# Kernel tuning notes

Hardware: AMD Instinct MI355X
Metric: run time of the kernel (lower is better)

The kernel has to match this reference:

```python
import jax, jax.numpy as jnp
import numpy as np

N = 4096      # nodes
DIM = 256     # in/out channels
H = 8         # heads
C = DIM       # per-head channels (PyG TransformerConv: out_channels per head)
EPS = 1e-5    # LayerNorm eps
P_EDGE = 0.01 # adjacency density -> avg in-degree ~41


def setup_inputs() -> dict:
    key = jax.random.key(0)
    ks = jax.random.split(key, 12)
    x = jax.random.normal(ks[0], (1, N, DIM), jnp.float32)
    # sparse random graph encoded densely (dense_to_sparse extracts nonzeros)
    adj_mat = (jax.random.uniform(ks[1], (1, N, N)) < P_EDGE).astype(jnp.float32)
    s = 1.0 / np.sqrt(DIM)
    Wq = jax.random.normal(ks[2], (DIM, H * C), jnp.float32) * s
    Wk = jax.random.normal(ks[3], (DIM, H * C), jnp.float32) * s
    Wv = jax.random.normal(ks[4], (DIM, H * C), jnp.float32) * s
    bq = jax.random.normal(ks[5], (H * C,), jnp.float32) * 0.01
    bk = jax.random.normal(ks[6], (H * C,), jnp.float32) * 0.01
    bv = jax.random.normal(ks[7], (H * C,), jnp.float32) * 0.01
    Wskip = jax.random.normal(ks[8], (DIM, DIM), jnp.float32) * s
    bskip = jax.random.normal(ks[9], (DIM,), jnp.float32) * 0.01
    gamma = jnp.ones((DIM,), jnp.float32)
    beta = jnp.zeros((DIM,), jnp.float32)
    return dict(x=x, adj_mat=adj_mat, Wq=Wq, bq=bq, Wk=Wk, bk=bk, Wv=Wv, bv=bv,
                Wskip=Wskip, bskip=bskip, gamma=gamma, beta=beta)


def reference(x, adj_mat, Wq, bq, Wk, bk, Wv, bv, Wskip, bskip, gamma, beta):
    xs = x[0]            # [N, DIM]
    adj = adj_mat[0]     # [N, N]; adj[j, i] != 0 => edge j -> i (source_to_target)
    q = (xs @ Wq + bq).reshape(N, H, C)
    k = (xs @ Wk + bk).reshape(N, H, C)
    v = (xs @ Wv + bv).reshape(N, H, C)
    # scaled dot-product attention restricted to graph edges
    scores = jnp.einsum('ihc,jhc->hij', q, k) / jnp.sqrt(jnp.float32(C))  # [H,N,N]
    mask = (adj.T != 0.0)[None]  # [1, i_target, j_source]
    neg = jnp.finfo(scores.dtype).min
    attn = jax.nn.softmax(jnp.where(mask, scores, neg), axis=-1)
    # nodes with no in-edges aggregate zero messages (scatter semantics)
    has_nbr = mask.any(axis=-1, keepdims=True)  # [1, N, 1]
    attn = jnp.where(has_nbr, attn, 0.0)
    agg = jnp.einsum('hij,jhc->ihc', attn, v)  # [N, H, C]
    out = agg.mean(axis=1)                      # concat=False -> head mean, [N, DIM]
    out = out + xs @ Wskip + bskip              # root_weight skip connection
    mu = out.mean(axis=-1, keepdims=True)
    var = ((out - mu) ** 2).mean(axis=-1, keepdims=True)
    out = (out - mu) * jax.lax.rsqrt(var + EPS) * gamma + beta  # LayerNorm
    out = out + xs                               # residual
    return out[None]  # [1, N, DIM]
```

## Files before the change

kernel.cpp:

```cpp
#include <hip/hip_runtime.h>
#include <hip/hip_bf16.h>

#define NN   4096
#define DIMM 256
#define HH   8
#define HC   2048
#define CAP  128

#define QSCALE 15.875f
#define SSCALE (0.0625f / (QSCALE * QSCALE))
#define V4SCALE 1.75f
#define V4INV  (4.0f / 7.0f)
#define V4CORR (32.0f / 7.0f)

typedef short    bf16x8 __attribute__((ext_vector_type(8)));
typedef float    f32x4  __attribute__((ext_vector_type(4)));

__device__ __forceinline__ unsigned short f2bf(float f) {
  union { float f; unsigned int u; } un; un.f = f;
  unsigned int r = un.u + 0x7fffu + ((un.u >> 16) & 1u);
  return (unsigned short)(r >> 16);
}
__device__ __forceinline__ int sdot4(unsigned int a, unsigned int b, int c) {
#if __has_builtin(__builtin_amdgcn_sdot4)
  return __builtin_amdgcn_sdot4((int)a, (int)b, c, false);
#else
  c += (int)(signed char)(a)       * (int)(signed char)(b);
  c += (int)(signed char)(a >> 8)  * (int)(signed char)(b >> 8);
  c += (int)(signed char)(a >> 16) * (int)(signed char)(b >> 16);
  c += (int)(signed char)(a >> 24) * (int)(signed char)(b >> 24);
  return c;
#endif
}
__device__ __forceinline__ void gload16(const void* g, void* l) {
  __builtin_amdgcn_global_load_lds(
      (const __attribute__((address_space(1))) unsigned int*)g,
      (__attribute__((address_space(3))) unsigned int*)l, 16, 0, 0);
}
__device__ __forceinline__ unsigned int pack8n(unsigned int a, unsigned int b) {
  const unsigned int ya = a | (a >> 4);
  const unsigned int yb = b | (b >> 4);
  return (ya & 0xFFu) | ((ya >> 8) & 0xFF00u) |
         (((yb & 0xFFu) | ((yb >> 8) & 0xFF00u)) << 16);
}

__global__ __launch_bounds__(256) void build_edges_kernel(
    const float4* __restrict__ adj4, int* __restrict__ deg, int* __restrict__ nbr) {
  const int stride = gridDim.x * blockDim.x;
  for (int e4 = blockIdx.x * blockDim.x + threadIdx.x; e4 < NN * NN / 4; e4 += stride) {
    const float4 a = adj4[e4];
    if (a.x != 0.f || a.y != 0.f || a.z != 0.f || a.w != 0.f) {
      const int e = e4 << 2;
      const int j = e >> 12;
      const int ib = e & (NN - 1);
      if (a.x != 0.f) { int s = atomicAdd(&deg[ib + 0], 1); if (s < CAP) nbr[(ib + 0) * CAP + s] = j; }
      if (a.y != 0.f) { int s = atomicAdd(&deg[ib + 1], 1); if (s < CAP) nbr[(ib + 1) * CAP + s] = j; }
      if (a.z != 0.f) { int s = atomicAdd(&deg[ib + 2], 1); if (s < CAP) nbr[(ib + 2) * CAP + s] = j; }
      if (a.w != 0.f) { int s = atomicAdd(&deg[ib + 3], 1); if (s < CAP) nbr[(ib + 3) * CAP + s] = j; }
    }
  }
}

__global__ __launch_bounds__(128) void sort_nbr_kernel(
    const int* __restrict__ deg, int* __restrict__ nbr) {
  const int i = blockIdx.x, t = threadIdx.x;
  __shared__ int sl[CAP];
  int d = deg[i];
  if (d > CAP) d = CAP;
  if (d <= 1) return;
  sl[t] = (t < d) ? nbr[i * CAP + t] : 0x7fffffff;
  __syncthreads();
  for (int ksz = 2; ksz <= CAP; ksz <<= 1) {
    for (int jsz = ksz >> 1; jsz > 0; jsz >>= 1) {
      const int ixj = t ^ jsz;
      if (ixj > t) {
        const int a = sl[t], b = sl[ixj];
        const bool up = ((t & ksz) == 0);
        if ((up && a > b) || (!up && a < b)) { sl[t] = b; sl[ixj] = a; }
      }
      __syncthreads();
    }
  }
  if (t < d) nbr[i * CAP + t] = sl[t];
}

__global__ __launch_bounds__(256) void cast_x_kernel(
    const float* __restrict__ x, unsigned short* __restrict__ xb) {
  const int gid = blockIdx.x * 256 + threadIdx.x;
  const int m = gid >> 5, c = gid & 31;
  const float4 a = *(const float4*)&x[(size_t)m * 256 + c * 8];
  const float4 b = *(const float4*)&x[(size_t)m * 256 + c * 8 + 4];
  union { unsigned short u[8]; uint4 v; } o;
  o.u[0] = f2bf(a.x); o.u[1] = f2bf(a.y); o.u[2] = f2bf(a.z); o.u[3] = f2bf(a.w);
  o.u[4] = f2bf(b.x); o.u[5] = f2bf(b.y); o.u[6] = f2bf(b.z); o.u[7] = f2bf(b.w);
  const int cs = (c & 24) | ((c & 7) ^ (m & 7));
  *(uint4*)&xb[(size_t)m * 256 + cs * 8] = o.v;
}

__global__ __launch_bounds__(256) void tcast_w_kernel(
    const float* __restrict__ W0, const float* __restrict__ W1,
    const float* __restrict__ W2, unsigned short* __restrict__ T0,
    unsigned short* __restrict__ T1, unsigned short* __restrict__ T2, int Nw) {
  const float* W = blockIdx.z == 0 ? W0 : blockIdx.z == 1 ? W1 : W2;
  unsigned short* T = blockIdx.z == 0 ? T0 : blockIdx.z == 1 ? T1 : T2;
  __shared__ float Tf[64][68];
  const int t = threadIdx.x;
  const int n0 = blockIdx.x * 64, k0 = blockIdx.y * 64;
  const int kk0 = t >> 4, nc = t & 15;
#pragma unroll
  for (int r = 0; r < 4; ++r) {
    const int kk = kk0 + r * 16;
    const float4 a = *(const float4*)&W[(size_t)(k0 + kk) * Nw + n0 + nc * 4];
    Tf[kk][nc * 4 + 0] = a.x; Tf[kk][nc * 4 + 1] = a.y;
    Tf[kk][nc * 4 + 2] = a.z; Tf[kk][nc * 4 + 3] = a.w;
  }
  __syncthreads();
  const int n = t >> 2, cp = t & 3;
#pragma unroll
  for (int qq = 0; qq < 2; ++qq) {
    const int cc = cp * 2 + qq;
    union { unsigned short u[8]; uint4 v; } o;
#pragma unroll
    for (int e = 0; e < 8; ++e) o.u[e] = f2bf(Tf[cc * 8 + e][n]);
    const int ng = n0 + n;
    const int co = cc ^ (ng & 7);
    *(uint4*)&T[(size_t)ng * 256 + blockIdx.y * 64 + co * 8] = o.v;
  }
}

__global__ __launch_bounds__(256) void mfma_gemm_kernel(
    const unsigned short* __restrict__ Abf,
    const unsigned short* __restrict__ B0, const unsigned short* __restrict__ B1,
    const unsigned short* __restrict__ B2, const unsigned short* __restrict__ B3,
    const float* __restrict__ bias0, const float* __restrict__ bias1,
    const float* __restrict__ bias2, const float* __restrict__ bias3,
    void* __restrict__ C0v, void* __restrict__ C1v,
    void* __restrict__ C2v, void* __restrict__ C3v) {
  const int z = blockIdx.z;
  if (z == 3 && blockIdx.x >= 2) return;
  const unsigned short* Bm = z == 0 ? B0 : z == 1 ? B1 : z == 2 ? B2 : B3;
  const float* bias = z == 0 ? bias0 : z == 1 ? bias1 : z == 2 ? bias2 : bias3;
  void* Cv = z == 0 ? C0v : z == 1 ? C1v : z == 2 ? C2v : C3v;
  const int Nc = (z == 3) ? 256 : 2048;

  __shared__ unsigned short lds[2 * 128 * 64];
  unsigned short* As = lds;
  unsigned short* Bs = lds + 128 * 64;

  const int t = threadIdx.x, l = t & 63, w = t >> 6;
  const int m0 = blockIdx.y * 128, n0 = blockIdx.x * 128;
  const int wm = w >> 1, wn = w & 1;

  const f32x4 zero = {0.f, 0.f, 0.f, 0.f};
  f32x4 acc[4][4];
#pragma unroll
  for (int fm = 0; fm < 4; ++fm)
#pragma unroll
    for (int fn = 0; fn < 4; ++fn) acc[fm][fn] = zero;

  for (int kb = 0; kb < 4; ++kb) {
#pragma unroll
    for (int r = 0; r < 4; ++r) {
      const int rr = r * 8 + (l >> 3), ch = l & 7;
      gload16(Abf + (size_t)(m0 + w * 32 + rr) * 256 + kb * 64 + ch * 8,
              As + w * 2048 + r * 512);
      gload16(Bm + (size_t)(n0 + w * 32 + rr) * 256 + kb * 64 + ch * 8,
              Bs + w * 2048 + r * 512);
    }
    __syncthreads();

#pragma unroll
    for (int s = 0; s < 2; ++s) {
      const int chab = (4 * s + (l >> 4)) ^ (l & 7);
      bf16x8 af[4], bfr[4];
#pragma unroll
      for (int fm = 0; fm < 4; ++fm) {
        const int row = wm * 64 + fm * 16 + (l & 15);
        af[fm] = *(const bf16x8*)&As[row * 64 + chab * 8];
      }
#pragma unroll
      for (int fn = 0; fn < 4; ++fn) {
        const int row = wn * 64 + fn * 16 + (l & 15);
        bfr[fn] = *(const bf16x8*)&Bs[row * 64 + chab * 8];
      }
#pragma unroll
      for (int fm = 0; fm < 4; ++fm)
#pragma unroll
        for (int fn = 0; fn < 4; ++fn)
          acc[fm][fn] = __builtin_amdgcn_mfma_f32_16x16x32_bf16(
              af[fm], bfr[fn], acc[fm][fn], 0, 0, 0);
    }
    __syncthreads();
  }

  float bv[4];
#pragma unroll
  for (int fn = 0; fn < 4; ++fn) bv[fn] = bias[n0 + wn * 64 + fn * 16 + (l & 15)];

  if (z < 2) {
    unsigned char* lds8 = (unsigned char*)lds;
    unsigned char* Cc8 = (unsigned char*)Cv;
#pragma unroll
    for (int fm = 0; fm < 4; ++fm) {
      const int col = wn * 64 + (l & 15);
#pragma unroll
      for (int fn = 0; fn < 4; ++fn) {
#pragma unroll
        for (int r = 0; r < 4; ++r) {
          const int row = wm * 64 + fm * 16 + (l >> 4) * 4 + r;
          const float val = acc[fm][fn][r] + bv[fn];
          int vi = (int)rintf(val * QSCALE);
          vi = vi < -127 ? -127 : (vi > 127 ? 127 : vi);
          lds8[row * 128 + col + fn * 16] = (unsigned char)(signed char)vi;
        }
      }
    }
    __syncthreads();
#pragma unroll
    for (int r2 = 0; r2 < 4; ++r2) {
      const int idx = r2 * 256 + t;
      const int row = idx >> 3, colb = (idx & 7) * 16;
      *(uint4*)&Cc8[(size_t)(m0 + row) * Nc + n0 + colb] =
          *(const uint4*)&lds8[row * 128 + colb];
    }
  } else if (z == 2) {
    unsigned char* lds8 = (unsigned char*)lds;
    unsigned char* Cc8 = (unsigned char*)Cv;
#pragma unroll
    for (int fm = 0; fm < 4; ++fm) {
      const int col = wn * 64 + (l & 15);
#pragma unroll
      for (int fn = 0; fn < 4; ++fn) {
#pragma unroll
        for (int r = 0; r < 4; ++r) {
          const int row = wm * 64 + fm * 16 + (l >> 4) * 4 + r;
          const float val = acc[fm][fn][r] + bv[fn];
          int vi = (int)rintf(val * V4SCALE) + 8;
          vi = vi < 0 ? 0 : (vi > 15 ? 15 : vi);
          lds8[row * 128 + col + fn * 16] = (unsigned char)vi;
        }
      }
    }
    __syncthreads();
#pragma unroll
    for (int u2 = 0; u2 < 2; ++u2) {
      const int unit = u2 * 256 + t;
      const int row = unit >> 2, ch = unit & 3;
      const uint4 x0 = *(const uint4*)&lds8[row * 128 + ch * 32];
      const uint4 x1 = *(const uint4*)&lds8[row * 128 + ch * 32 + 16];
      uint4 o;
      o.x = pack8n(x0.x, x0.y); o.y = pack8n(x0.z, x0.w);
      o.z = pack8n(x1.x, x1.y); o.w = pack8n(x1.z, x1.w);
      *(uint4*)&Cc8[(size_t)(m0 + row) * 1024 + (n0 >> 1) + ch * 16] = o;
    }
  } else {
    float* Cc = (float*)Cv;
#pragma unroll
    for (int fm = 0; fm < 4; ++fm)
#pragma unroll
      for (int fn = 0; fn < 4; ++fn)
#pragma unroll
        for (int r = 0; r < 4; ++r) {
          const int row = wm * 64 + fm * 16 + (l >> 4) * 4 + r;
          const int col = wn * 64 + fn * 16 + (l & 15);
          Cc[(size_t)(m0 + row) * Nc + n0 + col] = acc[fm][fn][r] + bv[fn];
        }
  }
}

__global__ __launch_bounds__(256) void attn_ln_kernel(
    const unsigned char* __restrict__ q8, const unsigned char* __restrict__ k8,
    const unsigned char* __restrict__ v4, const float* __restrict__ skip,
    const float* __restrict__ x, const int* __restrict__ deg,
    const int* __restrict__ nbr, const float* __restrict__ gamma,
    const float* __restrict__ beta, float* __restrict__ out) {
  const int i = blockIdx.x;
  const int t = threadIdx.x;
  const int lane = t & 63, wave = t >> 6;
  const int h = lane >> 3, sub = lane & 7;

  __shared__ int slist[CAP];
  __shared__ float sc[CAP * HH];
  __shared__ float wacc[4][2][DIMM];
  __shared__ float mred[HH], lred[HH];
  __shared__ float w1[4], w2[4];

  int d = deg[i];
  if (d > CAP) d = CAP;

  if (t < CAP) slist[t] = (t < d) ? nbr[i * CAP + t] : 0;

  uint4 Q0, Q1;
  {
    const uint4* qp = (const uint4*)&q8[(size_t)i * HC + (h << 8) + (sub << 5)];
    Q0 = qp[0]; Q1 = qp[1];
  }
  __syncthreads();

  {
    const size_t hoff = (size_t)(h << 8) + (sub << 5);
    int n = wave;
    uint4 a0, a1, b0, b1;
    if (n < d) {
      const uint4* kp = (const uint4*)&k8[(size_t)slist[n] * HC + hoff];
      a0 = kp[0]; a1 = kp[1];
    }
    if (n + 4 < d) {
      const uint4* kp = (const uint4*)&k8[(size_t)slist[n + 4] * HC + hoff];
      b0 = kp[0]; b1 = kp[1];
    }
    while (n < d) {
      uint4 c0, c1;
      if (n + 8 < d) {
        const uint4* kp = (const uint4*)&k8[(size_t)slist[n + 8] * HC + hoff];
        c0 = kp[0]; c1 = kp[1];
      }
      int iacc = 0;
      iacc = sdot4(a0.x, Q0.x, iacc); iacc = sdot4(a0.y, Q0.y, iacc);
      iacc = sdot4(a0.z, Q0.z, iacc); iacc = sdot4(a0.w, Q0.w, iacc);
      iacc = sdot4(a1.x, Q1.x, iacc); iacc = sdot4(a1.y, Q1.y, iacc);
      iacc = sdot4(a1.z, Q1.z, iacc); iacc = sdot4(a1.w, Q1.w, iacc);
      float s = (float)iacc;
      s += __shfl_xor(s, 1);
      s += __shfl_xor(s, 2);
      s += __shfl_xor(s, 4);
      if (sub == 0) sc[n * HH + h] = s * SSCALE;
      a0 = b0; a1 = b1; b0 = c0; b1 = c1;
      n += 4;
    }
  }
  __syncthreads();

  if (t < 64) {
    const int h2i = t >> 3, s2 = t & 7;
    float m = -1e30f;
    for (int n2 = s2; n2 < d; n2 += 8) m = fmaxf(m, sc[n2 * HH + h2i]);
    m = fmaxf(m, __shfl_xor(m, 1));
    m = fmaxf(m, __shfl_xor(m, 2));
    m = fmaxf(m, __shfl_xor(m, 4));
    float lsum = 0.f;
    for (int n2 = s2; n2 < d; n2 += 8) lsum += expf(sc[n2 * HH + h2i] - m);
    lsum += __shfl_xor(lsum, 1);
    lsum += __shfl_xor(lsum, 2);
    lsum += __shfl_xor(lsum, 4);
    if (s2 == 0) { mred[h2i] = m; lred[h2i] = (lsum > 0.f) ? V4INV / lsum : 0.f; }
  }
  __syncthreads();

  for (int e = t; e < d * HH; e += 256) {
    const int hh = e & (HH - 1);
    sc[e] = expf(sc[e] - mred[hh]) * lred[hh];
  }
  __syncthreads();

  float a[8] = {0.f, 0.f, 0.f, 0.f, 0.f, 0.f, 0.f, 0.f};
  const int g = lane >> 5, c8 = lane & 31;
  {
    const size_t voff = (size_t)(g * 4) * 128 + (size_t)c8 * 4;
    int n = wave;
    unsigned int A0, A1, A2, A3, B0w, B1w, B2w, B3w;
    if (n < d) {
      const unsigned char* vr = &v4[(size_t)slist[n] * 1024 + voff];
      A0 = *(const unsigned int*)(vr + 0 * 128); A1 = *(const unsigned int*)(vr + 1 * 128);
      A2 = *(const unsigned int*)(vr + 2 * 128); A3 = *(const unsigned int*)(vr + 3 * 128);
    }
    if (n + 4 < d) {
      const unsigned char* vr = &v4[(size_t)slist[n + 4] * 1024 + voff];
      B0w = *(const unsigned int*)(vr + 0 * 128); B1w = *(const unsigned int*)(vr + 1 * 128);
      B2w = *(const unsigned int*)(vr + 2 * 128); B3w = *(const unsigned int*)(vr + 3 * 128);
    }
    while (n < d) {
      unsigned int C0, C1, C2, C3;
      if (n + 8 < d) {
        const unsigned char* vr = &v4[(size_t)slist[n + 8] * 1024 + voff];
        C0 = *(const unsigned int*)(vr + 0 * 128); C1 = *(const unsigned int*)(vr + 1 * 128);
        C2 = *(const unsigned int*)(vr + 2 * 128); C3 = *(const unsigned int*)(vr + 3 * 128);
      }
      const float p0 = sc[n * HH + g * 4 + 0];
      const float p1 = sc[n * HH + g * 4 + 1];
      const float p2 = sc[n * HH + g * 4 + 2];
      const float p3 = sc[n * HH + g * 4 + 3];
#define AGG4(w, p)                                                     \
      {                                                                \
        const unsigned int lo = (w) & 0x0F0F0F0Fu;                     \
        const unsigned int hi = ((w) >> 4) & 0x0F0F0F0Fu;              \
        a[0] = fmaf(p, (float)(lo & 0xFFu), a[0]);                     \
        a[1] = fmaf(p, (float)(hi & 0xFFu), a[1]);                     \
        a[2] = fmaf(p, (float)((lo >> 8) & 0xFFu), a[2]);              \
        a[3] = fmaf(p, (float)((hi >> 8) & 0xFFu), a[3]);              \
        a[4] = fmaf(p, (float)((lo >> 16) & 0xFFu), a[4]);             \
        a[5] = fmaf(p, (float)((hi >> 16) & 0xFFu), a[5]);             \
        a[6] = fmaf(p, (float)(lo >> 24), a[6]);                       \
        a[7] = fmaf(p, (float)(hi >> 24), a[7]);                       \
      }
      AGG4(A0, p0) AGG4(A1, p1) AGG4(A2, p2) AGG4(A3, p3)
#undef AGG4
      A0 = B0w; A1 = B1w; A2 = B2w; A3 = B3w;
      B0w = C0; B1w = C1; B2w = C2; B3w = C3;
      n += 4;
    }
  }
#pragma unroll
  for (int e = 0; e < 8; ++e) wacc[wave][g][c8 * 8 + e] = a[e];
  __syncthreads();

  float accsum = 0.f;
#pragma unroll
  for (int w2 = 0; w2 < 4; ++w2) accsum += wacc[w2][0][t] + wacc[w2][1][t];
  const float corr = (d > 0) ? V4CORR : 0.f;
  const float oval = accsum * 0.125f - corr + skip[(size_t)i * DIMM + t];

  float s1 = oval, s2 = oval * oval;
#pragma unroll
  for (int off = 32; off > 0; off >>= 1) {
    s1 += __shfl_xor(s1, off, 64);
    s2 += __shfl_xor(s2, off, 64);
  }
  if (lane == 0) { w1[wave] = s1; w2[wave] = s2; }
  __syncthreads();
  const float S1 = w1[0] + w1[1] + w1[2] + w1[3];
  const float S2 = w2[0] + w2[1] + w2[2] + w2[3];
  const float mu = S1 * (1.0f / 256.0f);
  const float var = S2 * (1.0f / 256.0f) - mu * mu;
  const float rst = rsqrtf(var + 1e-5f);

  out[(size_t)i * DIMM + t] =
      (oval - mu) * rst * gamma[t] + beta[t] + x[(size_t)i * DIMM + t];
}

extern "C" void kernel_launch(void* const* d_in, const int* in_sizes, int n_in,
                              void* d_out, int out_size, void* d_ws, size_t ws_size,
                              hipStream_t stream) {
  const float* x     = (const float*)d_in[0];
  const float* adj   = (const float*)d_in[1];
  const float* Wq    = (const float*)d_in[2];
  const float* bq    = (const float*)d_in[3];
  const float* Wk    = (const float*)d_in[4];
  const float* bk    = (const float*)d_in[5];
  const float* Wv    = (const float*)d_in[6];
  const float* bv    = (const float*)d_in[7];
  const float* Wskip = (const float*)d_in[8];
  const float* bskip = (const float*)d_in[9];
  const float* gamma = (const float*)d_in[10];
  const float* beta  = (const float*)d_in[11];
  float* out = (float*)d_out;

  char* ws = (char*)d_ws;
  unsigned short* xb  = (unsigned short*)ws;
  unsigned short* WqT = xb  + (size_t)NN * DIMM;
  unsigned short* WkT = WqT + (size_t)HC * DIMM;
  unsigned short* WvT = WkT + (size_t)HC * DIMM;
  unsigned short* WsT = WvT + (size_t)HC * DIMM;
  float* skip = (float*)(WsT + (size_t)DIMM * DIMM);
  unsigned char* q8 = (unsigned char*)(skip + (size_t)NN * DIMM);
  unsigned char* k8 = q8 + (size_t)NN * HC;
  unsigned char* v4 = k8 + (size_t)NN * HC;
  int* deg = (int*)(v4 + (size_t)NN * 1024);
  int* nbr = deg + NN;

  hipMemsetAsync(deg, 0, NN * sizeof(int), stream);
  build_edges_kernel<<<2048, 256, 0, stream>>>((const float4*)adj, deg, nbr);
  sort_nbr_kernel<<<NN, 128, 0, stream>>>(deg, nbr);

  cast_x_kernel<<<NN * 32 / 256, 256, 0, stream>>>(x, xb);
  tcast_w_kernel<<<dim3(HC / 64, 4, 3), 256, 0, stream>>>(Wq, Wk, Wv, WqT, WkT, WvT, HC);
  tcast_w_kernel<<<dim3(DIMM / 64, 4, 1), 256, 0, stream>>>(Wskip, Wskip, Wskip,
                                                            WsT, WsT, WsT, DIMM);

  mfma_gemm_kernel<<<dim3(HC / 128, NN / 128, 4), 256, 0, stream>>>(
      xb, WqT, WkT, WvT, WsT, bq, bk, bv, bskip, q8, k8, v4, skip);

  attn_ln_kernel<<<NN, 256, 0, stream>>>(q8, k8, v4, skip, x, deg, nbr,
                                         gamma, beta, out);
}
```

Before: 139.7 us.

## Relayout packed V for 16-byte gathers and fold memset and cast launches

Changes the 4-bit V storage layout so that each lane's four heads for its eight channels are contiguous. The aggregation loop can then fetch one 16-byte load per neighbour instead of four scattered 4-byte loads, and the prefetch depth grows from two to three neighbours ahead. It also drops the separate hipMemsetAsync by zeroing deg inside cast_x_kernel, and merges the two weight transpose launches into one. The GEMM epilogue now does narrower 4-byte scattered stores, and the extra prefetch adds register pressure.

Measured after the change: 136.8 us. 1.02x faster.

```diff
diff --git a/kernel.cpp b/kernel.cpp
--- a/kernel.cpp
+++ b/kernel.cpp
@@ -85,7 +85,9 @@
 }
 
 __global__ __launch_bounds__(256) void cast_x_kernel(
-    const float* __restrict__ x, unsigned short* __restrict__ xb) {
+    const float* __restrict__ x, unsigned short* __restrict__ xb,
+    int* __restrict__ deg) {
+  if (blockIdx.x < 16) deg[blockIdx.x * 256 + threadIdx.x] = 0;
   const int gid = blockIdx.x * 256 + threadIdx.x;
   const int m = gid >> 5, c = gid & 31;
   const float4 a = *(const float4*)&x[(size_t)m * 256 + c * 8];
@@ -99,10 +101,14 @@
 
 __global__ __launch_bounds__(256) void tcast_w_kernel(
     const float* __restrict__ W0, const float* __restrict__ W1,
-    const float* __restrict__ W2, unsigned short* __restrict__ T0,
-    unsigned short* __restrict__ T1, unsigned short* __restrict__ T2, int Nw) {
-  const float* W = blockIdx.z == 0 ? W0 : blockIdx.z == 1 ? W1 : W2;
-  unsigned short* T = blockIdx.z == 0 ? T0 : blockIdx.z == 1 ? T1 : T2;
+    const float* __restrict__ W2, const float* __restrict__ W3,
+    unsigned short* __restrict__ T0, unsigned short* __restrict__ T1,
+    unsigned short* __restrict__ T2, unsigned short* __restrict__ T3) {
+  const int z = blockIdx.z;
+  if (z == 3 && blockIdx.x >= 4) return;
+  const float* W = z == 0 ? W0 : z == 1 ? W1 : z == 2 ? W2 : W3;
+  unsigned short* T = z == 0 ? T0 : z == 1 ? T1 : z == 2 ? T2 : T3;
+  const int Nw = (z == 3) ? 256 : 2048;
   __shared__ float Tf[64][68];
   const int t = threadIdx.x;
   const int n0 = blockIdx.x * 64, k0 = blockIdx.y * 64;
@@ -242,16 +248,16 @@
       }
     }
     __syncthreads();
-#pragma unroll
-    for (int u2 = 0; u2 < 2; ++u2) {
-      const int unit = u2 * 256 + t;
-      const int row = unit >> 2, ch = unit & 3;
-      const uint4 x0 = *(const uint4*)&lds8[row * 128 + ch * 32];
-      const uint4 x1 = *(const uint4*)&lds8[row * 128 + ch * 32 + 16];
-      uint4 o;
-      o.x = pack8n(x0.x, x0.y); o.y = pack8n(x0.z, x0.w);
-      o.z = pack8n(x1.x, x1.y); o.w = pack8n(x1.z, x1.w);
-      *(uint4*)&Cc8[(size_t)(m0 + row) * 1024 + (n0 >> 1) + ch * 16] = o;
+    const int hd = n0 >> 8, g2 = hd >> 2, hrel = hd & 3;
+    const int c8base = (n0 & 255) >> 3;
+#pragma unroll
+    for (int u = 0; u < 8; ++u) {
+      const int unit = u * 256 + t;
+      const int row = unit >> 4, c8r = unit & 15;
+      const uint2 x0 = *(const uint2*)&lds8[row * 128 + c8r * 8];
+      const unsigned int pk = pack8n(x0.x, x0.y);
+      *(unsigned int*)&Cc8[(size_t)(m0 + row) * 1024 + g2 * 512 +
+                           (c8base + c8r) * 16 + hrel * 4] = pk;
     }
   } else {
     float* Cc = (float*)Cv;
@@ -356,26 +362,15 @@
   float a[8] = {0.f, 0.f, 0.f, 0.f, 0.f, 0.f, 0.f, 0.f};
   const int g = lane >> 5, c8 = lane & 31;
   {
-    const size_t voff = (size_t)(g * 4) * 128 + (size_t)c8 * 4;
+    const size_t voff = (size_t)g * 512 + (size_t)c8 * 16;
     int n = wave;
-    unsigned int A0, A1, A2, A3, B0w, B1w, B2w, B3w;
-    if (n < d) {
-      const unsigned char* vr = &v4[(size_t)slist[n] * 1024 + voff];
-      A0 = *(const unsigned int*)(vr + 0 * 128); A1 = *(const unsigned int*)(vr + 1 * 128);
-      A2 = *(const unsigned int*)(vr + 2 * 128); A3 = *(const unsigned int*)(vr + 3 * 128);
-    }
-    if (n + 4 < d) {
-      const unsigned char* vr = &v4[(size_t)slist[n + 4] * 1024 + voff];
-      B0w = *(const unsigned int*)(vr + 0 * 128); B1w = *(const unsigned int*)(vr + 1 * 128);
-      B2w = *(const unsigned int*)(vr + 2 * 128); B3w = *(const unsigned int*)(vr + 3 * 128);
-    }
+    uint4 A, B, C;
+    if (n < d)     A = *(const uint4*)&v4[(size_t)slist[n] * 1024 + voff];
+    if (n + 4 < d) B = *(const uint4*)&v4[(size_t)slist[n + 4] * 1024 + voff];
+    if (n + 8 < d) C = *(const uint4*)&v4[(size_t)slist[n + 8] * 1024 + voff];
     while (n < d) {
-      unsigned int C0, C1, C2, C3;
-      if (n + 8 < d) {
-        const unsigned char* vr = &v4[(size_t)slist[n + 8] * 1024 + voff];
-        C0 = *(const unsigned int*)(vr + 0 * 128); C1 = *(const unsigned int*)(vr + 1 * 128);
-        C2 = *(const unsigned int*)(vr + 2 * 128); C3 = *(const unsigned int*)(vr + 3 * 128);
-      }
+      uint4 Dw;
+      if (n + 12 < d) Dw = *(const uint4*)&v4[(size_t)slist[n + 12] * 1024 + voff];
       const float p0 = sc[n * HH + g * 4 + 0];
       const float p1 = sc[n * HH + g * 4 + 1];
       const float p2 = sc[n * HH + g * 4 + 2];
@@ -393,10 +388,9 @@
         a[6] = fmaf(p, (float)(lo >> 24), a[6]);                       \
         a[7] = fmaf(p, (float)(hi >> 24), a[7]);                       \
       }
-      AGG4(A0, p0) AGG4(A1, p1) AGG4(A2, p2) AGG4(A3, p3)
+      AGG4(A.x, p0) AGG4(A.y, p1) AGG4(A.z, p2) AGG4(A.w, p3)
 #undef AGG4
-      A0 = B0w; A1 = B1w; A2 = B2w; A3 = B3w;
-      B0w = C0; B1w = C1; B2w = C2; B3w = C3;
+      A = B; B = C; C = Dw;
       n += 4;
     }
   }
@@ -458,14 +452,12 @@
   int* deg = (int*)(v4 + (size_t)NN * 1024);
   int* nbr = deg + NN;
 
-  hipMemsetAsync(deg, 0, NN * sizeof(int), stream);
+  cast_x_kernel<<<NN * 32 / 256, 256, 0, stream>>>(x, xb, deg);
   build_edges_kernel<<<2048, 256, 0, stream>>>((const float4*)adj, deg, nbr);
   sort_nbr_kernel<<<NN, 128, 0, stream>>>(deg, nbr);
 
-  cast_x_kernel<<<NN * 32 / 256, 256, 0, stream>>>(x, xb);
-  tcast_w_kernel<<<dim3(HC / 64, 4, 3), 256, 0, stream>>>(Wq, Wk, Wv, WqT, WkT, WvT, HC);
-  tcast_w_kernel<<<dim3(DIMM / 64, 4, 1), 256, 0, stream>>>(Wskip, Wskip, Wskip,
-                                                            WsT, WsT, WsT, DIMM);
+  tcast_w_kernel<<<dim3(HC / 64, 4, 4), 256, 0, stream>>>(
+      Wq, Wk, Wv, Wskip, WqT, WkT, WvT, WsT);
 
   mfma_gemm_kernel<<<dim3(HC / 128, NN / 128, 4), 256, 0, stream>>>(
       xb, WqT, WkT, WvT, WsT, bq, bk, bv, bskip, q8, k8, v4, skip);
```
